# Optimization experiments

Measured on AMD Instinct MI355X. Metric: run time of the kernel, lower is better.

Reference implementation:

```python
import jax, jax.numpy as jnp
import numpy as np

K = 8          # number of nearest neighbors (init kwarg k)
EPS = 1e-16    # torch_geometric clamps squared distance at 1e-16


def setup_inputs() -> dict:
    key = jax.random.key(0)
    k1, k2, k3, k4 = jax.random.split(key, 4)
    N, D, B = 16384, 128, 64
    x1 = jax.random.normal(k1, (N, 3 + D), dtype=jnp.float32)  # true graph: [coords(3) | feats(D)]
    x2 = jax.random.normal(k2, (N, 3 + D), dtype=jnp.float32)  # pred graph
    b1 = jnp.sort(jax.random.randint(k3, (N,), 0, B))          # sorted per-node graph ids
    b2 = jnp.sort(jax.random.randint(k4, (N,), 0, B))
    return {"x1": x1, "x2": x2, "b1": b1, "b2": b2}


def _knn_interpolate(f1, c1, c2, b1, b2, k):
    # Squared pairwise distances [N2, N1] via ||a||^2 + ||b||^2 - 2ab (GEMM form).
    d2 = (jnp.sum(c2 * c2, axis=-1)[:, None]
          + jnp.sum(c1 * c1, axis=-1)[None, :]
          - 2.0 * (c2 @ c1.T))
    d2 = jnp.maximum(d2, 0.0)
    # Batch-aware kNN: forbid cross-graph neighbors.
    d2 = jnp.where(b2[:, None] != b1[None, :], jnp.inf, d2)
    neg_d2, idx = jax.lax.top_k(-d2, k)          # k smallest distances per target node
    w = 1.0 / jnp.clip(-neg_d2, EPS)             # [N2, k] inverse-squared-distance weights
    nbr = f1[idx]                                # [N2, k, D] gather of neighbor features
    return jnp.einsum('nk,nkd->nd', w, nbr) / jnp.sum(w, axis=-1, keepdims=True)


def reference(x1, x2, b1, b2):
    c1, f1 = x1[:, :3], x1[:, 3:]
    c2, f2 = x2[:, :3], x2[:, 3:]
    f1_interp = _knn_interpolate(f1, c1, c2, b1, b2, K)
    return jnp.mean((f1_interp - f2) ** 2)
```

## Files before the change

### kernel.cpp

```cpp
#include <hip/hip_runtime.h>
#include <math.h>

#define KNN 8
#define QPB 32
#define SUB 16
#define BLK 512
#define CAP 512

__launch_bounds__(BLK, 4)
__global__ void knn_one(const float* __restrict__ x1,
                        const float* __restrict__ x2,
                        const int* __restrict__ b1,
                        const int* __restrict__ b2,
                        int N, int ROW, float scale,
                        unsigned long long* __restrict__ slot,
                        float* __restrict__ out) {
  __shared__ float4 c4[2][CAP];
  __shared__ int   bs[2][CAP];
  __shared__ int   s_info[2];
  __shared__ float wred[BLK / 64];

  const int nwg = (int)gridDim.x;
  const int xcd = (int)blockIdx.x & 7, pos = (int)blockIdx.x >> 3;
  const int q8 = nwg >> 3, r8 = nwg & 7;
  const int bid = (xcd < r8) ? xcd * (q8 + 1) + pos
                             : r8 * (q8 + 1) + (xcd - r8) * q8 + pos;

  const int tid  = threadIdx.x;
  const int lane = tid & 63;
  const int wv   = tid >> 6;
  const int qi   = tid >> 4;
  const int sub  = tid & (SUB - 1);
  const int q0   = bid * QPB;
  const int q    = min(q0 + qi, N - 1);
  const int qlast = min(q0 + QPB - 1, N - 1);

  float qx, qy, qz; int mybatch;
  float f2v[KNN];
  {
    const float* c2 = x2 + (size_t)q * ROW;
    qx = c2[0]; qy = c2[1]; qz = c2[2];
    mybatch = b2[q];
    const float* f2 = c2 + 3 + sub;
#pragma unroll
    for (int t = 0; t < KNN; ++t) f2v[t] = f2[16 * t];
  }

  if (wv < 2) {
    const int bb = (wv == 0) ? b2[q0] : b2[qlast];
    const int target = bb + wv;
    int lo = 0, hi = N;
    while (lo < hi) {
      int step = (hi - lo + 63) >> 6;
      int p = lo + lane * step;
      bool pred = (p < hi) && (b1[p] < target);
      int c = __popcll(__ballot(pred));
      if (c == 0) { hi = lo; break; }
      int nlo = lo + (c - 1) * step + 1;
      hi = min(hi, lo + c * step);
      lo = nlo;
    }
    if (lane == 0) s_info[wv] = lo;
  }

  unsigned long long K[KNN];
  const unsigned long long KINIT = 0x7F800000ULL << 32;
#pragma unroll
  for (int k = 0; k < KNN; ++k) K[k] = KINIT;

  __syncthreads();
  const int s1v = s_info[0], e1v = s_info[1];

  int t0 = s1v, t1 = min(t0 + CAP, e1v), buf = 0;
  {
    int i = t0 + tid;
    if (i < t1) {
      const float* p = x1 + (size_t)i * ROW;
      c4[0][i - t0] = make_float4(p[0], p[1], p[2], 0.f);
      bs[0][i - t0] = b1[i];
    }
  }
  __syncthreads();

  while (true) {
    const int tn0 = t1, tn1 = min(tn0 + CAP, e1v);
    float nx = 0.f, ny = 0.f, nz = 0.f; int nb = 0;
    const bool have_next = tn0 < e1v;
    const int ni = tn0 + tid;
    if (have_next && ni < tn1) {
      const float* p = x1 + (size_t)ni * ROW;
      nx = p[0]; ny = p[1]; nz = p[2]; nb = b1[ni];
    }
    for (int j = t0 + sub; j < t1; j += SUB) {
      float4 c = c4[buf][j - t0];
      int bv = bs[buf][j - t0];
      float dx = qx - c.x, dy = qy - c.y, dz = qz - c.z;
      float d = fmaf(dx, dx, fmaf(dy, dy, dz * dz));
      unsigned long long key =
          ((unsigned long long)__float_as_uint(d) << 32) | (unsigned)j;
      key = (bv == mybatch) ? key : ~0ULL;
      bool lt[KNN];
#pragma unroll
      for (int k = 0; k < KNN; ++k) lt[k] = key < K[k];
#pragma unroll
      for (int k = KNN - 1; k > 0; --k)
        K[k] = lt[k - 1] ? K[k - 1] : (lt[k] ? key : K[k]);
      K[0] = lt[0] ? key : K[0];
    }
    if (!have_next) break;
    if (ni < tn1) {
      c4[buf ^ 1][ni - tn0] = make_float4(nx, ny, nz, 0.f);
      bs[buf ^ 1][ni - tn0] = nb;
    }
    __syncthreads();
    t0 = tn0; t1 = tn1; buf ^= 1;
  }

  float acc[KNN];
#pragma unroll
  for (int t = 0; t < KNN; ++t) acc[t] = 0.f;
  float sw = 0.f;
  const float* x1f = x1 + 3 + sub;
#pragma unroll
  for (int r = 0; r < KNN; ++r) {
    unsigned long long h = K[0], b = h;
#pragma unroll
    for (int m = 1; m <= 8; m <<= 1) {
      unsigned long long o = __shfl_xor(b, m);
      b = (o < b) ? o : b;
    }
    if (h == b) {
#pragma unroll
      for (int k = 0; k < KNN - 1; ++k) K[k] = K[k + 1];
      K[KNN - 1] = KINIT;
    }
    float bd = __uint_as_float((unsigned)(b >> 32));
    int   bi = (int)(unsigned)b;
    float w = 1.0f / fmaxf(bd, 1e-16f);
    sw += w;
    const float* f = x1f + (size_t)bi * ROW;
#pragma unroll
    for (int t = 0; t < KNN; ++t) acc[t] = fmaf(w, f[16 * t], acc[t]);
  }

  float pacc = 0.0f;
  if (q0 + qi < N) {
    float rinv = 1.0f / sw;
#pragma unroll
    for (int t = 0; t < KNN; ++t) {
      float e = fmaf(acc[t], rinv, -f2v[t]);
      pacc += e * e;
    }
  }
#pragma unroll
  for (int off = 32; off > 0; off >>= 1) pacc += __shfl_xor(pacc, off);
  if (lane == 0) wred[wv] = pacc;
  __syncthreads();

  if (tid == 0) {
    float s = 0.0f;
#pragma unroll
    for (int w = 0; w < BLK / 64; ++w) s += wred[w];
    unsigned long long v =
        ((unsigned long long)(0x5A000000u | (unsigned)bid) << 32) |
        (unsigned long long)__float_as_uint(s);
    __hip_atomic_store(&slot[bid], v, __ATOMIC_RELAXED,
                       __HIP_MEMORY_SCOPE_AGENT);
  }

  if (bid == 0 && wv == 0) {
    float s = 0.0f;
    for (int r = 0; r * 64 + lane < nwg; ++r) {
      int i = r * 64 + lane;
      unsigned tag = 0x5A000000u | (unsigned)i;
      unsigned long long x = __hip_atomic_load(&slot[i], __ATOMIC_RELAXED,
                                               __HIP_MEMORY_SCOPE_AGENT);
      while ((unsigned)(x >> 32) != tag) {
        __builtin_amdgcn_s_sleep(8);
        x = __hip_atomic_load(&slot[i], __ATOMIC_RELAXED,
                              __HIP_MEMORY_SCOPE_AGENT);
      }
      s += __uint_as_float((unsigned)x);
    }
#pragma unroll
    for (int off = 32; off > 0; off >>= 1) s += __shfl_xor(s, off);
    if (lane == 0) out[0] = s * scale;
  }
}

extern "C" void kernel_launch(void* const* d_in, const int* in_sizes, int n_in,
                              void* d_out, int out_size, void* d_ws, size_t ws_size,
                              hipStream_t stream) {
  const float* x1 = (const float*)d_in[0];
  const float* x2 = (const float*)d_in[1];
  const int* b1 = (const int*)d_in[2];
  const int* b2 = (const int*)d_in[3];
  int N = in_sizes[2];
  int ROW = in_sizes[0] / N;
  float* out = (float*)d_out;

  int blocks = (N + QPB - 1) / QPB;
  unsigned long long* slot = (unsigned long long*)d_ws;
  if (ws_size < (size_t)blocks * sizeof(unsigned long long)) return;

  float scale = 1.0f / ((float)N * (float)(ROW - 3));
  knn_one<<<blocks, BLK, 0, stream>>>(x1, x2, b1, b2, N, ROW, scale, slot, out);
}
```

Baseline: 25.17 us.

## Halve queries per block, drop double buffering, pack batch id into float4

Blocks now hold 16 queries with 256 threads, and the grid doubles. The double-buffered candidate tile is replaced by a single 768-entry tile filled with a strided loop. The batch id is packed into the w component of the coordinate float4, so each candidate needs one LDS read instead of two. This trades prefetch overlap for less shared memory, more blocks and fewer LDS loads. The extra blocks each rescan their batch's candidates and add more partial sums to the final reduction.

```diff
diff --git a/kernel.cpp b/kernel.cpp
--- a/kernel.cpp
+++ b/kernel.cpp
@@ -2,10 +2,10 @@
 #include <math.h>
 
 #define KNN 8
-#define QPB 32
+#define QPB 16
 #define SUB 16
-#define BLK 512
-#define CAP 512
+#define BLK 256
+#define CAP 768
 
 __launch_bounds__(BLK, 4)
 __global__ void knn_one(const float* __restrict__ x1,
@@ -15,8 +15,7 @@
                         int N, int ROW, float scale,
                         unsigned long long* __restrict__ slot,
                         float* __restrict__ out) {
-  __shared__ float4 c4[2][CAP];
-  __shared__ int   bs[2][CAP];
+  __shared__ float4 c4[CAP];
   __shared__ int   s_info[2];
   __shared__ float wred[BLK / 64];
 
@@ -71,34 +70,21 @@
   __syncthreads();
   const int s1v = s_info[0], e1v = s_info[1];
 
-  int t0 = s1v, t1 = min(t0 + CAP, e1v), buf = 0;
-  {
-    int i = t0 + tid;
-    if (i < t1) {
+  for (int t0 = s1v; t0 < e1v; t0 += CAP) {
+    const int t1 = min(t0 + CAP, e1v);
+    __syncthreads();
+    for (int i = t0 + tid; i < t1; i += BLK) {
       const float* p = x1 + (size_t)i * ROW;
-      c4[0][i - t0] = make_float4(p[0], p[1], p[2], 0.f);
-      bs[0][i - t0] = b1[i];
+      c4[i - t0] = make_float4(p[0], p[1], p[2], __int_as_float(b1[i]));
     }
-  }
-  __syncthreads();
-
-  while (true) {
-    const int tn0 = t1, tn1 = min(tn0 + CAP, e1v);
-    float nx = 0.f, ny = 0.f, nz = 0.f; int nb = 0;
-    const bool have_next = tn0 < e1v;
-    const int ni = tn0 + tid;
-    if (have_next && ni < tn1) {
-      const float* p = x1 + (size_t)ni * ROW;
-      nx = p[0]; ny = p[1]; nz = p[2]; nb = b1[ni];
-    }
+    __syncthreads();
     for (int j = t0 + sub; j < t1; j += SUB) {
-      float4 c = c4[buf][j - t0];
-      int bv = bs[buf][j - t0];
+      float4 c = c4[j - t0];
       float dx = qx - c.x, dy = qy - c.y, dz = qz - c.z;
       float d = fmaf(dx, dx, fmaf(dy, dy, dz * dz));
       unsigned long long key =
           ((unsigned long long)__float_as_uint(d) << 32) | (unsigned)j;
-      key = (bv == mybatch) ? key : ~0ULL;
+      key = (__float_as_int(c.w) == mybatch) ? key : ~0ULL;
       bool lt[KNN];
 #pragma unroll
       for (int k = 0; k < KNN; ++k) lt[k] = key < K[k];
@@ -107,13 +93,6 @@
         K[k] = lt[k - 1] ? K[k - 1] : (lt[k] ? key : K[k]);
       K[0] = lt[0] ? key : K[0];
     }
-    if (!have_next) break;
-    if (ni < tn1) {
-      c4[buf ^ 1][ni - tn0] = make_float4(nx, ny, nz, 0.f);
-      bs[buf ^ 1][ni - tn0] = nb;
-    }
-    __syncthreads();
-    t0 = tn0; t1 = tn1; buf ^= 1;
   }
 
   float acc[KNN];
@@ -158,9 +137,7 @@
   __syncthreads();
 
   if (tid == 0) {
-    float s = 0.0f;
-#pragma unroll
-    for (int w = 0; w < BLK / 64; ++w) s += wred[w];
+    float s = (wred[0] + wred[1]) + (wred[2] + wred[3]);
     unsigned long long v =
         ((unsigned long long)(0x5A000000u | (unsigned)bid) << 32) |
         (unsigned long long)__float_as_uint(s);
```

After: 24.74 us. About the same (-1.7%).
